# Optimization experiments

Measured on AMD Instinct MI355X. Metric: run time of the kernel, lower is better.

Reference implementation:

```python
import jax, jax.numpy as jnp
import numpy as np

B, C, H, W = 64, 3, 64, 64
F = 96          # base_filters
K = 8           # n_mixtures
h, w = H // 2, W // 2
C0 = 2 * C      # channels of each checkerboard half
SECTIONS = [C0, C0, C0 * K, C0 * K, C0 * K]
SPLITS = [int(s) for s in np.cumsum(SECTIONS)[:-1]]
EPS = 1e-6


def conv2d(x, wgt, b):
    y = jax.lax.conv_general_dilated(x, wgt, (1, 1), 'SAME',
                                     dimension_numbers=('NCHW', 'OIHW', 'NCHW'))
    return y + b[None, :, None, None]


def layer_norm(x, g, b, eps=1e-5):
    # nn.LayerNorm(mid_shape): normalize over (C,H,W) per sample
    mu = jnp.mean(x, axis=(1, 2, 3), keepdims=True)
    var = jnp.var(x, axis=(1, 2, 3), keepdims=True)
    return (x - mu) / jnp.sqrt(var + eps) * g[None] + b[None]


def checker_split(z, odd=False):
    Bz, Cz, Hz, Wz = z.shape
    z = z.reshape(Bz, Cz, Hz // 2, 2, Wz // 2, 2)
    p00 = z[:, :, :, 0, :, 0]; p01 = z[:, :, :, 0, :, 1]
    p10 = z[:, :, :, 1, :, 0]; p11 = z[:, :, :, 1, :, 1]
    z0 = jnp.concatenate([p00, p11], axis=1)  # even checkerboard
    z1 = jnp.concatenate([p01, p10], axis=1)  # odd checkerboard
    if odd:
        z0, z1 = z1, z0
    return z0, z1


def checker_merge(z0, z1, odd=False):
    if odd:
        z0, z1 = z1, z0
    Cz = z0.shape[1] // 2
    p00, p11 = z0[:, :Cz], z0[:, Cz:]
    p01, p10 = z1[:, :Cz], z1[:, Cz:]
    Bz, _, hz, wz = p00.shape
    zi = jnp.stack([jnp.stack([p00, p01], axis=-1),
                    jnp.stack([p10, p11], axis=-1)], axis=-2)  # (B,C,h,w,2i,2j)
    z = zi.transpose(0, 1, 2, 4, 3, 5).reshape(Bz, Cz, 2 * hz, 2 * wz)
    return z


def gated_attn(x, qkv_w, qkv_b, proj_w, proj_b):
    Bx, Fx, hx, wx = x.shape
    xf = x.reshape(Bx, Fx, hx * wx).transpose(0, 2, 1)  # (B, L, F)
    qkv = xf @ qkv_w.T + qkv_b
    q, k, v = jnp.split(qkv, 3, axis=-1)
    scores = jnp.einsum('bqf,bkf->bqk', q, k) / jnp.sqrt(jnp.float32(Fx))
    attn = jax.nn.softmax(scores, axis=-1)
    o = jnp.einsum('bqk,bkf->bqf', attn, v)
    g = o @ proj_w.T + proj_b
    ga, gb = jnp.split(g, 2, axis=-1)
    out = xf + ga * jax.nn.sigmoid(gb)  # gated residual
    return out.transpose(0, 2, 1).reshape(Bx, Fx, hx, wx)


def conditioner(z1, conv1_w, conv1_b, gconv_w, gconv_b, ln1_g, ln1_b,
                qkv_w, qkv_b, proj_w, proj_b, ln2_g, ln2_b, conv2_w, conv2_b):
    x = conv2d(z1, conv1_w, conv1_b)
    g = conv2d(x, gconv_w, gconv_b)
    ga, gb = jnp.split(g, 2, axis=1)
    x = x + ga * jax.nn.sigmoid(gb)          # GatedConv2d
    x = layer_norm(x, ln1_g, ln1_b)
    x = gated_attn(x, qkv_w, qkv_b, proj_w, proj_b)
    x = layer_norm(x, ln2_g, ln2_b)
    return conv2d(x, conv2_w, conv2_b)


def _forward(z, log_df_dz, conv1_w, conv1_b, gconv_w, gconv_b, ln1_g, ln1_b,
             qkv_w, qkv_b, proj_w, proj_b, ln2_g, ln2_b, conv2_w, conv2_b,
             a_log_scale, a_bias):
    z0, z1 = checker_split(z)
    params = conditioner(z1, conv1_w, conv1_b, gconv_w, gconv_b, ln1_g, ln1_b,
                         qkv_w, qkv_b, proj_w, proj_b, ln2_g, ln2_b, conv2_w, conv2_b)
    a, b, logpi, mu, s = jnp.split(params, SPLITS, axis=1)
    a = jnp.tanh(a) * a_log_scale + a_bias
    Bz = z0.shape[0]
    logpi = jax.nn.log_softmax(logpi.reshape(Bz, K, C0, h, w), axis=1)
    mu = mu.reshape(Bz, K, C0, h, w)
    s = s.reshape(Bz, K, C0, h, w)
    # mixture-of-logistics CDF
    u = (z0[:, None] - mu) * jnp.exp(-s)
    x = jnp.sum(jnp.exp(logpi) * jax.nn.sigmoid(u), axis=1)
    log_pdf = jax.scipy.special.logsumexp(
        logpi - s + jax.nn.log_sigmoid(u) + jax.nn.log_sigmoid(-u), axis=1)
    log_df_dz = log_df_dz + jnp.sum(log_pdf.reshape(Bz, -1), axis=1)
    # logit transform
    x = jnp.clip(x, EPS, 1.0 - EPS)
    z0n = jnp.log(x) - jnp.log1p(-x)
    log_df_dz = log_df_dz + jnp.sum((-jnp.log(x) - jnp.log1p(-x)).reshape(Bz, -1), axis=1)
    # affine rescale
    z0n = z0n * jnp.exp(a) + b
    log_df_dz = log_df_dz + jnp.sum(a.reshape(Bz, -1), axis=1)
    return checker_merge(z0n, z1), log_df_dz


def setup_inputs() -> dict:
    key = jax.random.key(0)
    ks = jax.random.split(key, 10)
    sc = 0.05
    return dict(
        z=jax.random.normal(ks[0], (B, C, H, W), jnp.float32),
        log_df_dz=jnp.zeros((B,), jnp.float32),
        conv1_w=sc * jax.random.normal(ks[1], (F, C0, 3, 3), jnp.float32),
        conv1_b=jnp.zeros((F,), jnp.float32),
        gconv_w=sc * jax.random.normal(ks[2], (2 * F, F, 3, 3), jnp.float32),
        gconv_b=jnp.zeros((2 * F,), jnp.float32),
        ln1_g=jnp.ones((F, h, w), jnp.float32),
        ln1_b=jnp.zeros((F, h, w), jnp.float32),
        qkv_w=sc * jax.random.normal(ks[3], (3 * F, F), jnp.float32),
        qkv_b=jnp.zeros((3 * F,), jnp.float32),
        proj_w=sc * jax.random.normal(ks[4], (2 * F, F), jnp.float32),
        proj_b=jnp.zeros((2 * F,), jnp.float32),
        ln2_g=jnp.ones((F, h, w), jnp.float32),
        ln2_b=jnp.zeros((F, h, w), jnp.float32),
        conv2_w=sc * jax.random.normal(ks[5], (sum(SECTIONS), F, 3, 3), jnp.float32),
        conv2_b=jnp.zeros((sum(SECTIONS),), jnp.float32),
        a_log_scale=0.01 * jax.random.normal(ks[6], (1,), jnp.float32),
        a_bias=0.01 * jax.random.normal(ks[7], (1,), jnp.float32),
    )


def reference(z, log_df_dz, conv1_w, conv1_b, gconv_w, gconv_b, ln1_g, ln1_b,
              qkv_w, qkv_b, proj_w, proj_b, ln2_g, ln2_b, conv2_w, conv2_b,
              a_log_scale, a_bias):
    return _forward(z, log_df_dz, conv1_w, conv1_b, gconv_w, gconv_b, ln1_g, ln1_b,
                    qkv_w, qkv_b, proj_w, proj_b, ln2_g, ln2_b, conv2_w, conv2_b,
                    a_log_scale, a_bias)
```

## Files before the change

### kernel.cpp

```cpp
#include <hip/hip_runtime.h>
#include <cstdint>
#include <cstddef>


typedef unsigned short u16;
typedef __attribute__((ext_vector_type(8))) short short8;
typedef __attribute__((ext_vector_type(4))) float f32x4;
typedef __attribute__((ext_vector_type(4))) unsigned int u32x4;

__device__ __forceinline__ float sigm(float x){ return 1.0f/(1.0f+__expf(-x)); }

__device__ __forceinline__ u16 f2bf(float f){
    unsigned int u = __float_as_uint(f);
    u += 0x7fffu + ((u >> 16) & 1u);
    return (u16)(u >> 16);
}
__device__ __forceinline__ float bf2f(u16 v){
    unsigned int u = ((unsigned int)v) << 16;
    return __uint_as_float(u);
}

__device__ __forceinline__ void dma16(const u16* g, u16* l){
    __builtin_amdgcn_global_load_lds(
        (const __attribute__((address_space(1))) void*)g,
        (__attribute__((address_space(3))) void*)l,
        16, 0, 0);
}

__device__ __forceinline__ float ex2(float x){
    float r; asm("v_exp_f32 %0, %1" : "=v"(r) : "v"(x)); return r;
}
__device__ __forceinline__ unsigned cvtpk(float lo, float hi){
    unsigned r; asm("v_cvt_pk_bf16_f32 %0, %1, %2" : "=v"(r) : "v"(lo), "v"(hi)); return r;
}
__device__ __forceinline__ void plswap32(unsigned &a, unsigned &b){
    asm("v_permlane32_swap_b32 %0, %1" : "+v"(a), "+v"(b));
}
__device__ __forceinline__ void plswap16(unsigned &a, unsigned &b){
    asm("v_permlane16_swap_b32 %0, %1" : "+v"(a), "+v"(b));
}

#define SOFTPACK(S, LACC, PA) do { \
    unsigned pk_[4][2]; \
    _Pragma("unroll") \
    for (int t=0;t<4;++t){ \
        float e0 = ex2(S[t][0]); \
        float e1 = ex2(S[t][1]); \
        float e2 = ex2(S[t][2]); \
        float e3 = ex2(S[t][3]); \
        LACC += (e0+e1)+(e2+e3); \
        pk_[t][0] = cvtpk(e0,e1); \
        pk_[t][1] = cvtpk(e2,e3); \
    } \
    _Pragma("unroll") \
    for (int kk=0;kk<2;++kk){ \
        unsigned a0 = pk_[2*kk][0], b0 = pk_[2*kk+1][0]; \
        unsigned a1 = pk_[2*kk][1], b1 = pk_[2*kk+1][1]; \
        plswap32(a0,b0); plswap16(a0,b0); \
        plswap32(a1,b1); plswap16(a1,b1); \
        u32x4 dw_; dw_[0]=a0; dw_[1]=a1; dw_[2]=b0; dw_[3]=b1; \
        PA[kk] = __builtin_bit_cast(short8, dw_); \
    } \
} while(0)

__device__ __forceinline__ short8 ln_frag(const u16* __restrict__ xg,
    const float* __restrict__ gt, const float* __restrict__ bt,
    int p, int c0, float mu, float rr)
{
    short8 x8 = *reinterpret_cast<const short8*>(xg + (size_t)p*96 + c0);
    const float* gp = gt + (size_t)p*96 + c0;
    const float* bp = bt + (size_t)p*96 + c0;
    short8 o;
    #pragma unroll
    for (int j=0;j<8;++j){
        float ag = rr*gp[j];
        o[j] = (short)f2bf(bf2f((u16)x8[j])*ag + (bp[j] - mu*ag));
    }
    return o;
}

__global__ __launch_bounds__(256) void k_prep(
    const float* __restrict__ z, const float* __restrict__ c1w, const float* __restrict__ c1b,
    const float* __restrict__ gw, const float* __restrict__ c2w,
    const float* __restrict__ qkvw, const float* __restrict__ pw,
    const float* __restrict__ ln1g, const float* __restrict__ ln1b,
    const float* __restrict__ ln2g, const float* __restrict__ ln2b,
    const float* __restrict__ logdf,
    u16* __restrict__ x1b,
    u16* __restrict__ Wg, u16* __restrict__ W2,
    u16* __restrict__ Wqkv, u16* __restrict__ Wproj,
    float* __restrict__ gt1, float* __restrict__ bt1,
    float* __restrict__ gt2, float* __restrict__ bt2,
    float* __restrict__ outlog)
{
    int blk = blockIdx.x;
    int tid = threadIdx.x;
    __shared__ float tin[6][6][34];
    __shared__ __align__(16) u16 Wc[96][72];
    __shared__ __align__(16) u16 imc[128][72];

    if (blk < 512){
        int b  = blk >> 3;
        int pg = blk & 7;
        int r0 = pg*4;
        for (int e = tid; e < 96*72; e += 256){
            int oc = e/72, k = e%72;
            Wc[oc][k] = (k < 54) ? f2bf(c1w[oc*54 + k]) : (u16)0;
        }
        for (int idx = tid; idx < 6*6*34; idx += 256){
            int c = idx/204, rem = idx%204;
            int rr = rem/34, q = rem%34;
            int ii = r0 - 1 + rr, jj = q - 1;
            float v = 0.f;
            if ((unsigned)ii < 32u && (unsigned)jj < 32u){
                if (c < 3) v = z[((b*3+c)*64 + 2*ii)*64 + (2*jj+1)];
                else       v = z[((b*3+(c-3))*64 + (2*ii+1))*64 + 2*jj];
            }
            tin[c][rr][q] = v;
        }
        __syncthreads();
        for (int e = tid; e < 128*72; e += 256){
            int px = e/72, k = e%72;
            float v = 0.f;
            if (k < 54){
                int c = k/9, rr = (k%9)/3, dcc = k%3;
                v = tin[c][(px>>5)+rr][(px&31)+dcc];
            }
            imc[px][k] = f2bf(v);
        }
        __syncthreads();

        int w = tid >> 6, lane = tid & 63;
        int cc = lane & 15, gg = lane >> 4;
        f32x4 acc[2][6];
        #pragma unroll
        for (int u=0;u<2;++u)
            #pragma unroll
            for (int t=0;t<6;++t) acc[u][t] = (f32x4){0.f,0.f,0.f,0.f};

        #pragma unroll
        for (int ks=0; ks<2; ++ks){
            short8 a0 = *reinterpret_cast<const short8*>(&imc[w*32 + cc     ][ks*32 + 8*gg]);
            short8 a1 = *reinterpret_cast<const short8*>(&imc[w*32 + 16 + cc][ks*32 + 8*gg]);
            #pragma unroll
            for (int t=0; t<6; ++t){
                short8 bb = *reinterpret_cast<const short8*>(&Wc[t*16+cc][ks*32 + 8*gg]);
                acc[0][t] = __builtin_amdgcn_mfma_f32_16x16x32_bf16(a0, bb, acc[0][t], 0,0,0);
                acc[1][t] = __builtin_amdgcn_mfma_f32_16x16x32_bf16(a1, bb, acc[1][t], 0,0,0);
            }
        }

        #pragma unroll
        for (int u=0;u<2;++u){
            int p0 = pg*128 + w*32 + u*16 + gg*4;
            #pragma unroll
            for (int t=0;t<6;++t){
                int oc = t*16+cc;
                float bv = c1b[oc];
                #pragma unroll
                for (int r=0;r<4;++r)
                    x1b[((size_t)(b*1024) + p0 + r)*96 + oc] = f2bf(acc[u][t][r] + bv);
            }
        }
    } else if (blk < 1160){
        int idx = (blk-512)*256 + tid;
        int j = idx & 7;
        int lane = (idx >> 3) & 63;
        int fo = idx >> 9;
        int frag = fo % 18;
        int tob = fo / 18;
        int obk = tob & 1, tap = tob >> 1;
        int t = frag/3, ks = frag%3;
        int cc = lane & 15, gg = lane >> 4;
        int ocp = obk*96 + t*16 + cc;
        int r2 = ocp%96, isB = r2/48, i2 = r2%48;
        int oc = (ocp/96)*48 + i2 + isB*96;
        int ic = ks*32 + 8*gg + j;
        Wg[idx] = f2bf(gw[(size_t)(oc*96+ic)*9 + tap]);
    } else if (blk < 1700){
        int idx = (blk-1160)*256 + tid;
        int j = idx & 7;
        int lane = (idx >> 3) & 63;
        int fo = idx >> 9;
        int frag = fo % 15;
        int tob = fo / 15;
        int obk = tob & 1, tap = tob >> 1;
        int t = frag/3, ks = frag%3;
        int cc = lane & 15, gg = lane >> 4;
        int oc = obk*80 + t*16 + cc;
        int ic = ks*32 + 8*gg + j;
        W2[idx] = (oc < 156) ? f2bf(c2w[(size_t)(oc*96+ic)*9 + tap]) : (u16)0;
    } else if (blk < 1808){
        int idx = (blk-1700)*256 + tid;
        int j = idx & 7;
        int lane = (idx >> 3) & 63;
        int fo = idx >> 9;
        int frag = fo % 27;
        int obk = fo / 27;
        int t = frag/3, ks = frag%3;
        int cc = lane & 15, gg = lane >> 4;
        int n = obk*144 + t*16 + cc;
        int ic = ks*32 + 8*gg + j;
        Wqkv[idx] = f2bf(qkvw[(size_t)n*96 + ic]);
    } else if (blk < 1880){
        int idx = (blk-1808)*256 + tid;
        int j = idx & 7;
        int lane = (idx >> 3) & 63;
        int fo = idx >> 9;
        int frag = fo % 18;
        int obk = fo / 18;
        int t = frag/3, ks = frag%3;
        int cc = lane & 15, gg = lane >> 4;
        int ocp = obk*96 + t*16 + cc;
        int r2 = ocp%96, isB = r2/48, i2 = r2%48;
        int oc = obk*48 + i2 + isB*96;
        int ic = ks*32 + 8*gg + j;
        Wproj[idx] = f2bf(pw[(size_t)oc*96 + ic]);
    } else if (blk < 2264){
        int idx = (blk-1880)*256 + tid;
        int c = idx >> 10, p = idx & 1023;
        gt1[p*96 + c] = ln1g[idx];
    } else if (blk < 2648){
        int idx = (blk-2264)*256 + tid;
        int c = idx >> 10, p = idx & 1023;
        bt1[p*96 + c] = ln1b[idx];
    } else if (blk < 3032){
        int idx = (blk-2648)*256 + tid;
        int c = idx >> 10, p = idx & 1023;
        gt2[p*96 + c] = ln2g[idx];
    } else if (blk < 3416){
        int idx = (blk-3032)*256 + tid;
        int c = idx >> 10, p = idx & 1023;
        bt2[p*96 + c] = ln2b[idx];
    } else {
        if (tid < 64) outlog[tid] = logdf[tid];
    }
}

__global__ __launch_bounds__(256,4) void k_gconv(const u16* __restrict__ Xpb,
    const u16* __restrict__ Wt, const float* __restrict__ bias,
    u16* __restrict__ outb, float* __restrict__ partials)
{
    int blk  = blockIdx.x;
    int obk  = blk & 1;
    int pblk = (blk >> 1) & 7;
    int b    = blk >> 4;
    int tid  = threadIdx.x;
    int w = tid >> 6, lane = tid & 63;
    int cc = lane & 15, gg = lane >> 4;

    __shared__ __align__(16) u16 Ws[2][9216];
    __shared__ float red[8];

    f32x4 acc[2][6];
    #pragma unroll
    for (int u=0;u<2;++u)
        #pragma unroll
        for (int t=0;t<6;++t) acc[u][t] = (f32x4){0.f,0.f,0.f,0.f};

    int base = pblk*128 + w*32;
    int ia = base >> 5;
    const u16* xb = Xpb + (size_t)b*1024*96;

    {
        const u16* src = Wt + (size_t)obk*9216;
        #pragma unroll
        for (int i=0;i<5;++i){
            int c = tid + 256*i;
            if (c < 1152) dma16(src + (size_t)c*8, Ws[0] + (size_t)(w*64+256*i)*8);
        }
    }

    for (int tap=0; tap<9; ++tap){
        __syncthreads();
        if (tap < 8){
            const u16* src = Wt + (size_t)((tap+1)*2 + obk)*9216;
            int nb = (tap+1)&1;
            #pragma unroll
            for (int i=0;i<5;++i){
                int c = tid + 256*i;
                if (c < 1152) dma16(src + (size_t)c*8, Ws[nb] + (size_t)(w*64+256*i)*8);
            }
        }
        const u16* Wc = Ws[tap&1];
        int dr = tap/3 - 1, dc = tap%3 - 1;

        int ii = ia + dr;
        int jj0 = cc + dc, jj1 = cc + 16 + dc;
        bool rv = ((unsigned)ii < 32u);
        bool v0 = rv && ((unsigned)jj0 < 32u);
        bool v1 = rv && ((unsigned)jj1 < 32u);
        const u16* ar0 = xb + (ptrdiff_t)(ii*32 + jj0)*96 + 8*gg;
        const u16* ar1 = xb + (ptrdiff_t)(ii*32 + jj1)*96 + 8*gg;

        #pragma unroll
        for (int ks=0; ks<3; ++ks){
            short8 a0 = {0,0,0,0,0,0,0,0};
            short8 a1 = {0,0,0,0,0,0,0,0};
            if (v0) a0 = *reinterpret_cast<const short8*>(ar0 + ks*32);
            if (v1) a1 = *reinterpret_cast<const short8*>(ar1 + ks*32);
            #pragma unroll
            for (int t=0; t<6; ++t){
                short8 bb = *reinterpret_cast<const short8*>(Wc + ((size_t)(t*3+ks)*64 + lane)*8);
                acc[0][t] = __builtin_amdgcn_mfma_f32_16x16x32_bf16(a0, bb, acc[0][t], 0,0,0);
                acc[1][t] = __builtin_amdgcn_mfma_f32_16x16x32_bf16(a1, bb, acc[1][t], 0,0,0);
            }
        }
    }

    float s = 0.f, ssq = 0.f;
    #pragma unroll
    for (int u=0;u<2;++u){
        int p0 = base + u*16 + gg*4;
        #pragma unroll
        for (int t=0;t<3;++t){
            int ocA = obk*48 + t*16+cc;
            float ba = bias[ocA], bbv = bias[ocA+96];
            #pragma unroll
            for (int r=0;r<4;++r){
                float res = bf2f(Xpb[((size_t)b*1024 + p0+r)*96 + ocA]);
                float va = acc[u][t][r]   + ba;
                float vb = acc[u][t+3][r] + bbv;
                float v = res + va*sigm(vb);
                outb[((size_t)b*1024 + p0+r)*96 + ocA] = f2bf(v);
                s += v; ssq += v*v;
            }
        }
    }
    #pragma unroll
    for (int o=32;o>0;o>>=1){ s += __shfl_down(s,o,64); ssq += __shfl_down(ssq,o,64); }
    if (lane==0){ red[w]=s; red[4+w]=ssq; }
    __syncthreads();
    if (tid==0){
        int slot = b*16 + pblk*2 + obk;
        partials[slot*2+0] = red[0]+red[1]+red[2]+red[3];
        partials[slot*2+1] = red[4]+red[5]+red[6]+red[7];
    }
}

__global__ __launch_bounds__(256) void k_lne(const u16* __restrict__ xb,
    const float* __restrict__ gt, const float* __restrict__ bt,
    const float* __restrict__ partials, u16* __restrict__ out)
{
    int b = blockIdx.x / 48, rem = blockIdx.x % 48;
    float s=0.f, ss=0.f;
    #pragma unroll
    for (int i=0;i<16;++i){ s += partials[(b*16+i)*2]; ss += partials[(b*16+i)*2+1]; }
    float mu = s/98304.f;
    float r = rsqrtf(ss/98304.f - mu*mu + 1e-5f);

    int e8 = rem*256 + threadIdx.x;
    size_t base = (size_t)b*98304 + (size_t)e8*8;
    short8 x8 = *reinterpret_cast<const short8*>(xb + base);
    const float* gp = gt + e8*8;
    const float* bp = bt + e8*8;
    short8 o8;
    #pragma unroll
    for (int i=0;i<8;++i)
        o8[i] = (short)f2bf((bf2f((u16)x8[i]) - mu)*r*gp[i] + bp[i]);
    *reinterpret_cast<short8*>(out + base) = o8;
}

__global__ __launch_bounds__(256,4) void k_qkvm(const u16* __restrict__ Xg,
    const float* __restrict__ gt, const float* __restrict__ bt,
    const float* __restrict__ part,
    const u16* __restrict__ Wt, const float* __restrict__ bias,
    u16* __restrict__ Qb, u16* __restrict__ Kf, u16* __restrict__ Vf)
{
    int blk  = blockIdx.x;
    int obk  = blk & 1;
    int pblk = (blk >> 1) & 7;
    int b    = blk >> 4;
    int tid  = threadIdx.x;
    int w = tid >> 6, lane = tid & 63;
    int cc = lane & 15, gg = lane >> 4;
    const float scale = 0.14724445f;

    __shared__ __align__(16) u16 Ws[13824];
    {
        const u16* src = Wt + (size_t)obk*13824;
        #pragma unroll
        for (int i=0;i<7;++i){
            int c = tid + 256*i;
            if (c < 1728) dma16(src + (size_t)c*8, Ws + (size_t)(w*64+256*i)*8);
        }
    }

    float sS=0.f, sQ=0.f;
    #pragma unroll
    for (int i=0;i<16;++i){ sS += part[(b*16+i)*2]; sQ += part[(b*16+i)*2+1]; }
    float mu = sS/98304.f;
    float rr = rsqrtf(sQ/98304.f - mu*mu + 1e-5f);

    f32x4 acc[2][9];
    #pragma unroll
    for (int u=0;u<2;++u)
        #pragma unroll
        for (int t=0;t<9;++t) acc[u][t] = (f32x4){0.f,0.f,0.f,0.f};

    int base = pblk*128 + w*32;
    const u16* xg = Xg + (size_t)b*1024*96;
    __syncthreads();

    #pragma unroll
    for (int ks=0; ks<3; ++ks){
        int c0 = ks*32 + 8*gg;
        short8 a0 = ln_frag(xg, gt, bt, base+cc,    c0, mu, rr);
        short8 a1 = ln_frag(xg, gt, bt, base+cc+16, c0, mu, rr);
        #pragma unroll
        for (int t=0; t<9; ++t){
            short8 bb = *reinterpret_cast<const short8*>(Ws + ((size_t)(t*3+ks)*64 + lane)*8);
            acc[0][t] = __builtin_amdgcn_mfma_f32_16x16x32_bf16(a0, bb, acc[0][t], 0,0,0);
            acc[1][t] = __builtin_amdgcn_mfma_f32_16x16x32_bf16(a1, bb, acc[1][t], 0,0,0);
        }
    }

    #pragma unroll
    for (int u=0;u<2;++u){
        int p0 = base + u*16 + gg*4;
        #pragma unroll
        for (int t=0;t<9;++t){
            int n = obk*144 + t*16+cc;
            float bv = bias[n];
            #pragma unroll
            for (int r=0;r<4;++r){
                int p = p0 + r;
                float av = acc[u][t][r] + bv;
                if (n < 96){
                    Qb[((size_t)(b*1024+p))*96 + n] = f2bf(av*scale);
                } else if (n < 192){
                    int f = n-96;
                    int jt = p>>6, t16 = (p>>4)&3, ccs = p&15;
                    int ks = f>>5, ggs = (f>>3)&3, j = f&7;
                    Kf[(size_t)(b*16+jt)*6144 + (size_t)(((t16*3+ks)*4+ggs)*16+ccs)*8 + j] = f2bf(av);
                } else {
                    int f = n-192;
                    int jt = p>>6, kl = p&63;
                    int kk = kl>>5, ggs = (kl>>3)&3, j = kl&7;
                    int ft = f>>4, ccs = f&15;
                    Vf[(size_t)(b*16+jt)*6144 + (size_t)(((ft*2+kk)*4+ggs)*16+ccs)*8 + j] = f2bf(av);
                }
            }
        }
    }
}

__global__ __launch_bounds__(256,2) void k_attn(const u16* __restrict__ Qb,
    const u16* __restrict__ Kf, const u16* __restrict__ Vf, u16* __restrict__ Ob)
{
    int qt = blockIdx.x >> 6;
    int b  = blockIdx.x & 63;
    int tid = threadIdx.x;
    int w  = tid >> 6;
    int lane = tid & 63;
    int cc = lane & 15;
    int gg = lane >> 4;

    __shared__ __align__(16) u16 Ks[3][6144];
    __shared__ __align__(16) u16 Vs[3][6144];

    int q0 = qt*128 + w*32;

    short8 qf[2][3];
    {
        const u16* qr0 = Qb + ((size_t)(b*1024 + q0 + cc))*96;
        #pragma unroll
        for (int ks=0; ks<3; ++ks){
            qf[0][ks] = *reinterpret_cast<const short8*>(qr0 + ks*32 + 8*gg);
            qf[1][ks] = *reinterpret_cast<const short8*>(qr0 + (size_t)16*96 + ks*32 + 8*gg);
        }
    }

    f32x4 Oacc[2][6];
    #pragma unroll
    for (int u=0;u<2;++u)
        #pragma unroll
        for (int ft=0; ft<6; ++ft) Oacc[u][ft] = (f32x4){0.f,0.f,0.f,0.f};
    float l_acc[2] = {0.f, 0.f};

    const u16* Kb0 = Kf + (size_t)(b*16)*6144;
    const u16* Vb0 = Vf + (size_t)(b*16)*6144;

    #pragma unroll
    for (int i=0;i<3;++i){
        size_t c8 = (size_t)(tid + 256*i)*8;
        size_t l8 = (size_t)(w*64 + 256*i)*8;
        dma16(Kb0 + c8, Ks[0] + l8);
        dma16(Vb0 + c8, Vs[0] + l8);
    }
    #pragma unroll
    for (int i=0;i<3;++i){
        size_t c8 = (size_t)(6144 + (tid + 256*i)*8);
        size_t l8 = (size_t)(w*64 + 256*i)*8;
        dma16(Kb0 + c8, Ks[1] + l8);
        dma16(Vb0 + c8, Vs[1] + l8);
    }

    for (int jt=0; jt<16; ++jt){
        if (jt < 15) asm volatile("s_waitcnt vmcnt(6)" ::: "memory");
        else         asm volatile("s_waitcnt vmcnt(0)" ::: "memory");
        __builtin_amdgcn_s_barrier();
        __builtin_amdgcn_sched_barrier(0);

        if (jt < 14){
            const u16* kn = Kb0 + (size_t)(jt+2)*6144;
            const u16* vn = Vb0 + (size_t)(jt+2)*6144;
            u16* kd = Ks[(jt+2)%3];
            u16* vd = Vs[(jt+2)%3];
            #pragma unroll
            for (int i=0;i<3;++i){
                size_t c8 = (size_t)(tid + 256*i)*8;
                size_t l8 = (size_t)(w*64 + 256*i)*8;
                dma16(kn + c8, kd + l8);
                dma16(vn + c8, vd + l8);
            }
        }

        const u16* Kc = Ks[jt%3];
        const u16* Vc = Vs[jt%3];

        f32x4 S0[4], S1[4];
        #pragma unroll
        for (int t=0;t<4;++t){ S0[t] = (f32x4){0.f,0.f,0.f,0.f}; S1[t] = (f32x4){0.f,0.f,0.f,0.f}; }

        __builtin_amdgcn_s_setprio(1);
        #pragma unroll
        for (int ks=0; ks<3; ++ks){
            #pragma unroll
            for (int t=0; t<4; ++t){
                short8 kb = *reinterpret_cast<const short8*>(Kc + ((t*3+ks)*64 + lane)*8);
                S0[t] = __builtin_amdgcn_mfma_f32_16x16x32_bf16(kb, qf[0][ks], S0[t], 0,0,0);
                S1[t] = __builtin_amdgcn_mfma_f32_16x16x32_bf16(kb, qf[1][ks], S1[t], 0,0,0);
            }
        }
        __builtin_amdgcn_s_setprio(0);

        short8 pa0[2], pa1[2];
        SOFTPACK(S0, l_acc[0], pa0);
        SOFTPACK(S1, l_acc[1], pa1);

        __builtin_amdgcn_s_setprio(1);
        #pragma unroll
        for (int kk=0; kk<2; ++kk){
            #pragma unroll
            for (int ft=0; ft<6; ++ft){
                short8 vb = *reinterpret_cast<const short8*>(Vc + ((ft*2+kk)*64 + lane)*8);
                Oacc[0][ft] = __builtin_amdgcn_mfma_f32_16x16x32_bf16(pa0[kk], vb, Oacc[0][ft], 0,0,0);
                Oacc[1][ft] = __builtin_amdgcn_mfma_f32_16x16x32_bf16(pa1[kk], vb, Oacc[1][ft], 0,0,0);
            }
        }
        __builtin_amdgcn_s_setprio(0);
    }

    #pragma unroll
    for (int u=0;u<2;++u){
        float lv = l_acc[u];
        lv += __shfl_xor(lv, 16, 64);
        lv += __shfl_xor(lv, 32, 64);
        float linv[4];
        #pragma unroll
        for (int r=0;r<4;++r) linv[r] = 1.0f / __shfl(lv, 4*gg + r, 64);
        #pragma unroll
        for (int ft=0; ft<6; ++ft)
            #pragma unroll
            for (int r=0; r<4; ++r)
                Ob[((size_t)(b*1024 + q0 + u*16 + 4*gg + r))*96 + ft*16 + cc]
                    = f2bf(Oacc[u][ft][r]*linv[r]);
    }
}

__global__ __launch_bounds__(256,4) void k_projm(const u16* __restrict__ Opb,
    const u16* __restrict__ Wt, const float* __restrict__ bias,
    const u16* __restrict__ Xg, const float* __restrict__ gt, const float* __restrict__ bt,
    const float* __restrict__ part1,
    u16* __restrict__ outb, float* __restrict__ partials)
{
    int blk  = blockIdx.x;
    int obk  = blk & 1;
    int pblk = (blk >> 1) & 7;
    int b    = blk >> 4;
    int tid  = threadIdx.x;
    int w = tid >> 6, lane = tid & 63;
    int cc = lane & 15, gg = lane >> 4;

    __shared__ __align__(16) u16 Ws[9216];
    __shared__ float red[8];
    {
        const u16* src = Wt + (size_t)obk*9216;
        #pragma unroll
        for (int i=0;i<5;++i){
            int c = tid + 256*i;
            if (c < 1152) dma16(src + (size_t)c*8, Ws + (size_t)(w*64+256*i)*8);
        }
    }

    float sS=0.f, sQ=0.f;
    #pragma unroll
    for (int i=0;i<16;++i){ sS += part1[(b*16+i)*2]; sQ += part1[(b*16+i)*2+1]; }
    float mu1 = sS/98304.f;
    float rr1 = rsqrtf(sQ/98304.f - mu1*mu1 + 1e-5f);

    f32x4 acc[2][6];
    #pragma unroll
    for (int u=0;u<2;++u)
        #pragma unroll
        for (int t=0;t<6;++t) acc[u][t] = (f32x4){0.f,0.f,0.f,0.f};

    int base = pblk*128 + w*32;
    const u16* xb = Opb + ((size_t)b*1024 + base)*96;
    __syncthreads();

    #pragma unroll
    for (int ks=0; ks<3; ++ks){
        short8 a0 = *reinterpret_cast<const short8*>(xb + (size_t)cc*96      + ks*32 + 8*gg);
        short8 a1 = *reinterpret_cast<const short8*>(xb + (size_t)(cc+16)*96 + ks*32 + 8*gg);
        #pragma unroll
        for (int t=0; t<6; ++t){
            short8 bb = *reinterpret_cast<const short8*>(Ws + ((size_t)(t*3+ks)*64 + lane)*8);
            acc[0][t] = __builtin_amdgcn_mfma_f32_16x16x32_bf16(a0, bb, acc[0][t], 0,0,0);
            acc[1][t] = __builtin_amdgcn_mfma_f32_16x16x32_bf16(a1, bb, acc[1][t], 0,0,0);
        }
    }

    const u16* resb = Xg + (size_t)b*1024*96;
    float s = 0.f, ssq = 0.f;
    #pragma unroll
    for (int u=0;u<2;++u){
        int p0 = base + u*16 + gg*4;
        #pragma unroll
        for (int t=0;t<3;++t){
            int ocA = obk*48 + t*16+cc;
            float ba = bias[ocA], bbv = bias[ocA+96];
            #pragma unroll
            for (int r=0;r<4;++r){
                int pl = p0 + r;
                float ga = acc[u][t][r]   + ba;
                float gb = acc[u][t+3][r] + bbv;
                float xv = bf2f(resb[(size_t)pl*96 + ocA]);
                float res = (xv - mu1)*rr1*gt[(size_t)pl*96 + ocA] + bt[(size_t)pl*96 + ocA];
                float v = res + ga * sigm(gb);
                outb[((size_t)b*1024 + pl)*96 + ocA] = f2bf(v);
                s += v; ssq += v*v;
            }
        }
    }
    #pragma unroll
    for (int o=32;o>0;o>>=1){ s += __shfl_down(s,o,64); ssq += __shfl_down(ssq,o,64); }
    if (lane==0){ red[w]=s; red[4+w]=ssq; }
    __syncthreads();
    if (tid==0){
        int slot = b*16 + pblk*2 + obk;
        partials[slot*2+0] = red[0]+red[1]+red[2]+red[3];
        partials[slot*2+1] = red[4]+red[5]+red[6]+red[7];
    }
}

__global__ __launch_bounds__(256,2) void k_c2mix(const u16* __restrict__ Xpb,
    const u16* __restrict__ Wt, const float* __restrict__ bias,
    const float* __restrict__ z, const float* __restrict__ a_ls_p,
    const float* __restrict__ a_b_p, float* __restrict__ out_z, float* __restrict__ out_log)
{
    int blk  = blockIdx.x;
    int pblk = blk & 7;
    int b    = blk >> 3;
    int tid  = threadIdx.x;
    int w = tid >> 6, lane = tid & 63;
    int cc = lane & 15, gg = lane >> 4;

    __shared__ __align__(16) u16 SM[30720];
    __shared__ float red[4];

    f32x4 acc[2][10];
    #pragma unroll
    for (int u=0;u<2;++u)
        #pragma unroll
        for (int t=0;t<10;++t) acc[u][t] = (f32x4){0.f,0.f,0.f,0.f};

    int base = pblk*128 + w*32;
    int ia = base >> 5;
    const u16* xb = Xpb + (size_t)b*1024*96;

    {
        #pragma unroll
        for (int i=0;i<8;++i){
            int c = tid + 256*i;
            if (c < 1920) dma16(Wt + (size_t)c*8, SM + (size_t)(w*64+256*i)*8);
        }
    }

    for (int tap=0; tap<9; ++tap){
        __syncthreads();
        if (tap < 8){
            const u16* src = Wt + (size_t)(tap+1)*15360;
            u16* dst = SM + (size_t)((tap+1)&1)*15360;
            #pragma unroll
            for (int i=0;i<8;++i){
                int c = tid + 256*i;
                if (c < 1920) dma16(src + (size_t)c*8, dst + (size_t)(w*64+256*i)*8);
            }
        }
        const u16* Wc = SM + (size_t)(tap&1)*15360;
        int dr = tap/3 - 1, dc = tap%3 - 1;

        int ii = ia + dr;
        int jj0 = cc + dc, jj1 = cc + 16 + dc;
        bool rv = ((unsigned)ii < 32u);
        bool v0 = rv && ((unsigned)jj0 < 32u);
        bool v1 = rv && ((unsigned)jj1 < 32u);
        const u16* ar0 = xb + (ptrdiff_t)(ii*32 + jj0)*96 + 8*gg;
        const u16* ar1 = xb + (ptrdiff_t)(ii*32 + jj1)*96 + 8*gg;

        #pragma unroll
        for (int ks=0; ks<3; ++ks){
            short8 a0 = {0,0,0,0,0,0,0,0};
            short8 a1 = {0,0,0,0,0,0,0,0};
            if (v0) a0 = *reinterpret_cast<const short8*>(ar0 + ks*32);
            if (v1) a1 = *reinterpret_cast<const short8*>(ar1 + ks*32);
            #pragma unroll
            for (int t=0; t<10; ++t){
                int fl = (t<5) ? (t*3+ks) : (15 + (t-5)*3 + ks);
                short8 bb = *reinterpret_cast<const short8*>(Wc + ((size_t)fl*64 + lane)*8);
                acc[0][t] = __builtin_amdgcn_mfma_f32_16x16x32_bf16(a0, bb, acc[0][t], 0,0,0);
                acc[1][t] = __builtin_amdgcn_mfma_f32_16x16x32_bf16(a1, bb, acc[1][t], 0,0,0);
            }
        }
    }

    __syncthreads();
    #pragma unroll
    for (int u=0;u<2;++u){
        int lp0 = w*32 + u*16 + gg*4;
        #pragma unroll
        for (int t=0;t<10;++t){
            int oc = (t<5) ? (t*16+cc) : (80 + (t-5)*16 + cc);
            if (oc < 156){
                float bv = bias[oc];
                #pragma unroll
                for (int r=0;r<4;++r)
                    SM[oc*132 + lp0 + r] = f2bf(acc[u][t][r] + bv);
            }
        }
    }
    __syncthreads();

    float als = a_ls_p[0], abv = a_b_p[0];
    float logsum = 0.f;
    #pragma unroll
    for (int e3=0;e3<3;++e3){
        int e  = tid + 256*e3;
        int c0 = e >> 7, xp = e & 127;
        int pix = pblk*128 + xp;
        int i = pix >> 5, j = pix & 31;

        if (c0 < 3){
            int idx01 = ((b*3+c0)*64 + 2*i)*64 + 2*j+1;
            int idx10 = ((b*3+c0)*64 + 2*i+1)*64 + 2*j;
            out_z[idx01] = z[idx01];
            out_z[idx10] = z[idx10];
        }

        float z0v = (c0<3) ? z[((b*3+c0)*64 + 2*i)*64 + 2*j]
                           : z[((b*3+(c0-3))*64 + 2*i+1)*64 + 2*j+1];
        float a_raw = bf2f(SM[(c0)*132 + xp]);
        float bco   = bf2f(SM[(6+c0)*132 + xp]);
        float lpk[8], muk[8], svk[8];
        float m1 = -1e30f;
        #pragma unroll
        for (int k=0;k<8;++k){
            lpk[k] = bf2f(SM[(12 + k*6 + c0)*132 + xp]);
            muk[k] = bf2f(SM[(60 + k*6 + c0)*132 + xp]);
            svk[k] = bf2f(SM[(108 + k*6 + c0)*132 + xp]);
            m1 = fmaxf(m1, lpk[k]);
        }
        float se = 0.f;
        #pragma unroll
        for (int k=0;k<8;++k) se += __expf(lpk[k]-m1);
        float lse = m1 + __logf(se);
        float xm = 0.f, mt = -1e30f;
        float tk[8];
        #pragma unroll
        for (int k=0;k<8;++k){
            float lpn = lpk[k] - lse;
            float u = (z0v - muk[k]) * __expf(-svk[k]);
            float au = fabsf(u);
            xm += __expf(lpn) * (1.f/(1.f+__expf(-u)));
            float lss = -(au + 2.f*log1pf(__expf(-au)));
            float t2 = lpn - svk[k] + lss;
            tk[k] = t2; mt = fmaxf(mt, t2);
        }
        float se2 = 0.f;
        #pragma unroll
        for (int k=0;k<8;++k) se2 += __expf(tk[k]-mt);
        float logacc = mt + __logf(se2);
        xm = fminf(fmaxf(xm, 1e-6f), 1.f-1e-6f);
        float lx = __logf(xm), l1x = log1pf(-xm);
        logacc += -lx - l1x;
        float aa = tanhf(a_raw)*als + abv;
        float z0n = (lx - l1x)*__expf(aa) + bco;
        logacc += aa;
        int oidx = (c0<3) ? ((b*3+c0)*64 + 2*i)*64 + 2*j
                          : ((b*3+(c0-3))*64 + 2*i+1)*64 + 2*j+1;
        out_z[oidx] = z0n;
        logsum += logacc;
    }

    #pragma unroll
    for (int o=32;o>0;o>>=1) logsum += __shfl_down(logsum, o, 64);
    if (lane==0) red[w] = logsum;
    __syncthreads();
    if (tid==0) atomicAdd(out_log + b, red[0]+red[1]+red[2]+red[3]);
}

extern "C" void kernel_launch(void* const* d_in, const int* in_sizes, int n_in,
                              void* d_out, int out_size, void* d_ws, size_t ws_size,
                              hipStream_t stream)
{
    const float* z     = (const float*)d_in[0];
    const float* logdf = (const float*)d_in[1];
    const float* c1w   = (const float*)d_in[2];
    const float* c1b   = (const float*)d_in[3];
    const float* gw    = (const float*)d_in[4];
    const float* gcb   = (const float*)d_in[5];
    const float* ln1g  = (const float*)d_in[6];
    const float* ln1b  = (const float*)d_in[7];
    const float* qkvw  = (const float*)d_in[8];
    const float* qkvb  = (const float*)d_in[9];
    const float* pw    = (const float*)d_in[10];
    const float* pbb   = (const float*)d_in[11];
    const float* ln2g  = (const float*)d_in[12];
    const float* ln2b  = (const float*)d_in[13];
    const float* c2w   = (const float*)d_in[14];
    const float* c2b   = (const float*)d_in[15];
    const float* als   = (const float*)d_in[16];
    const float* ab    = (const float*)d_in[17];

    float* out_z   = (float*)d_out;
    float* out_log = out_z + 786432;

    float* ws     = (float*)d_ws;
    u16*   x1b    = (u16*)(ws + 0);
    u16*   xg_b   = (u16*)(ws + 3145728);
    u16*   Kf     = (u16*)(ws + 6291456);
    u16*   Vf     = (u16*)(ws + 9437184);
    u16*   Ob     = (u16*)(ws + 12582912);
    u16*   x2b    = (u16*)(ws + 15728640);
    u16*   Qb     = x1b;
    u16*   xln2b  = Kf;
    const size_t T = 19660800;
    float* gt1    = ws + T;
    float* bt1    = ws + T + 98304;
    float* gt2    = ws + T + 196608;
    float* bt2    = ws + T + 294912;
    float* part1  = ws + T + 393216;
    float* part2  = ws + T + 395264;
    u16*   Wg     = (u16*)(ws + T + 397568);
    u16*   W2     = (u16*)(ws + T + 480512);
    u16*   Wqkv   = (u16*)(ws + T + 549632);
    u16*   Wproj  = (u16*)(ws + T + 563456);

    k_prep   <<<3417, 256, 0, stream>>>(z, c1w, c1b, gw, c2w, qkvw, pw,
                                        ln1g, ln1b, ln2g, ln2b, logdf,
                                        x1b, Wg, W2, Wqkv, Wproj,
                                        gt1, bt1, gt2, bt2, out_log);
    k_gconv  <<<1024, 256, 0, stream>>>(x1b, Wg, gcb, xg_b, part1);
    k_qkvm   <<<1024, 256, 0, stream>>>(xg_b, gt1, bt1, part1, Wqkv, qkvb, Qb, Kf, Vf);
    k_attn   <<<512, 256, 0, stream>>>(Qb, Kf, Vf, Ob);
    k_projm  <<<1024, 256, 0, stream>>>(Ob, Wproj, pbb, xg_b, gt1, bt1, part1, x2b, part2);
    k_lne    <<<3072, 256, 0, stream>>>(x2b, gt2, bt2, part2, xln2b);
    k_c2mix  <<<512,  256, 0, stream>>>(xln2b, W2, c2b, z, als, ab, out_z, out_log);
}
```

Measured before the change: 256.2 us.

## Fuse attention with gated output projection and residual layernorm epilogue

Merges the attention kernel and the projection/gating kernel into one. The normalized attention output tile is kept in LDS (padded rows) instead of written to global and reread, and shared memory is reused for the full projection weight after the K/V loop. Each block now computes both output halves, so it holds 24 accumulator tiles and emits two partial-sum slots. This removes one launch and the global round trip of the attention output, but raises register pressure and serializes the projection behind the attention tail.

Result: faster. 247.0 us (median of 3 runs) (-3.6%).

```diff
diff --git a/kernel.cpp b/kernel.cpp
--- a/kernel.cpp
+++ b/kernel.cpp
@@ -445,8 +445,12 @@
     }
 }
 
-__global__ __launch_bounds__(256,2) void k_attn(const u16* __restrict__ Qb,
-    const u16* __restrict__ Kf, const u16* __restrict__ Vf, u16* __restrict__ Ob)
+__global__ __launch_bounds__(256,2) void k_attnproj(const u16* __restrict__ Qb,
+    const u16* __restrict__ Kf, const u16* __restrict__ Vf,
+    const u16* __restrict__ Wpg, const float* __restrict__ pbias,
+    const u16* __restrict__ Xg, const float* __restrict__ gt, const float* __restrict__ bt,
+    const float* __restrict__ part1,
+    u16* __restrict__ outb, float* __restrict__ partials)
 {
     int qt = blockIdx.x >> 6;
     int b  = blockIdx.x & 63;
@@ -456,8 +460,19 @@
     int cc = lane & 15;
     int gg = lane >> 4;
 
-    __shared__ __align__(16) u16 Ks[3][6144];
-    __shared__ __align__(16) u16 Vs[3][6144];
+    __shared__ __align__(16) u16 SM[36864];
+    __shared__ float red[16];
+
+    u16* Ksb = SM;
+    u16* Vsb = SM + 18432;
+    u16* Wp  = SM;
+    u16* Ot  = SM + 18432;
+
+    float sS=0.f, sQ=0.f;
+    #pragma unroll
+    for (int i=0;i<16;++i){ sS += part1[(b*16+i)*2]; sQ += part1[(b*16+i)*2+1]; }
+    float mu1 = sS/98304.f;
+    float rr1 = rsqrtf(sQ/98304.f - mu1*mu1 + 1e-5f);
 
     int q0 = qt*128 + w*32;
 
@@ -485,15 +500,15 @@
     for (int i=0;i<3;++i){
         size_t c8 = (size_t)(tid + 256*i)*8;
         size_t l8 = (size_t)(w*64 + 256*i)*8;
-        dma16(Kb0 + c8, Ks[0] + l8);
-        dma16(Vb0 + c8, Vs[0] + l8);
+        dma16(Kb0 + c8, Ksb + l8);
+        dma16(Vb0 + c8, Vsb + l8);
     }
     #pragma unroll
     for (int i=0;i<3;++i){
         size_t c8 = (size_t)(6144 + (tid + 256*i)*8);
         size_t l8 = (size_t)(w*64 + 256*i)*8;
-        dma16(Kb0 + c8, Ks[1] + l8);
-        dma16(Vb0 + c8, Vs[1] + l8);
+        dma16(Kb0 + c8, Ksb + 6144 + l8);
+        dma16(Vb0 + c8, Vsb + 6144 + l8);
     }
 
     for (int jt=0; jt<16; ++jt){
@@ -505,8 +520,8 @@
         if (jt < 14){
             const u16* kn = Kb0 + (size_t)(jt+2)*6144;
             const u16* vn = Vb0 + (size_t)(jt+2)*6144;
-            u16* kd = Ks[(jt+2)%3];
-            u16* vd = Vs[(jt+2)%3];
+            u16* kd = Ksb + (size_t)((jt+2)%3)*6144;
+            u16* vd = Vsb + (size_t)((jt+2)%3)*6144;
             #pragma unroll
             for (int i=0;i<3;++i){
                 size_t c8 = (size_t)(tid + 256*i)*8;
@@ -516,8 +531,8 @@
             }
         }
 
-        const u16* Kc = Ks[jt%3];
-        const u16* Vc = Vs[jt%3];
+        const u16* Kc = Ksb + (size_t)(jt%3)*6144;
+        const u16* Vc = Vsb + (size_t)(jt%3)*6144;
 
         f32x4 S0[4], S1[4];
         #pragma unroll
@@ -550,6 +565,14 @@
             }
         }
         __builtin_amdgcn_s_setprio(0);
+    }
+
+    __syncthreads();
+
+    #pragma unroll
+    for (int i=0;i<9;++i){
+        int c = tid + 256*i;
+        dma16(Wpg + (size_t)c*8, Wp + (size_t)(w*64+256*i)*8);
     }
 
     #pragma unroll
@@ -564,94 +587,69 @@
         for (int ft=0; ft<6; ++ft)
             #pragma unroll
             for (int r=0; r<4; ++r)
-                Ob[((size_t)(b*1024 + q0 + u*16 + 4*gg + r))*96 + ft*16 + cc]
+                Ot[(size_t)(w*32 + u*16 + 4*gg + r)*104 + ft*16 + cc]
                     = f2bf(Oacc[u][ft][r]*linv[r]);
     }
-}
-
-__global__ __launch_bounds__(256,4) void k_projm(const u16* __restrict__ Opb,
-    const u16* __restrict__ Wt, const float* __restrict__ bias,
-    const u16* __restrict__ Xg, const float* __restrict__ gt, const float* __restrict__ bt,
-    const float* __restrict__ part1,
-    u16* __restrict__ outb, float* __restrict__ partials)
-{
-    int blk  = blockIdx.x;
-    int obk  = blk & 1;
-    int pblk = (blk >> 1) & 7;
-    int b    = blk >> 4;
-    int tid  = threadIdx.x;
-    int w = tid >> 6, lane = tid & 63;
-    int cc = lane & 15, gg = lane >> 4;
-
-    __shared__ __align__(16) u16 Ws[9216];
-    __shared__ float red[8];
-    {
-        const u16* src = Wt + (size_t)obk*9216;
-        #pragma unroll
-        for (int i=0;i<5;++i){
-            int c = tid + 256*i;
-            if (c < 1152) dma16(src + (size_t)c*8, Ws + (size_t)(w*64+256*i)*8);
-        }
-    }
-
-    float sS=0.f, sQ=0.f;
-    #pragma unroll
-    for (int i=0;i<16;++i){ sS += part1[(b*16+i)*2]; sQ += part1[(b*16+i)*2+1]; }
-    float mu1 = sS/98304.f;
-    float rr1 = rsqrtf(sQ/98304.f - mu1*mu1 + 1e-5f);
-
-    f32x4 acc[2][6];
+
+    __syncthreads();
+
+    f32x4 pacc[2][12];
     #pragma unroll
     for (int u=0;u<2;++u)
         #pragma unroll
-        for (int t=0;t<6;++t) acc[u][t] = (f32x4){0.f,0.f,0.f,0.f};
-
-    int base = pblk*128 + w*32;
-    const u16* xb = Opb + ((size_t)b*1024 + base)*96;
-    __syncthreads();
+        for (int t=0;t<12;++t) pacc[u][t] = (f32x4){0.f,0.f,0.f,0.f};
 
     #pragma unroll
     for (int ks=0; ks<3; ++ks){
-        short8 a0 = *reinterpret_cast<const short8*>(xb + (size_t)cc*96      + ks*32 + 8*gg);
-        short8 a1 = *reinterpret_cast<const short8*>(xb + (size_t)(cc+16)*96 + ks*32 + 8*gg);
-        #pragma unroll
-        for (int t=0; t<6; ++t){
-            short8 bb = *reinterpret_cast<const short8*>(Ws + ((size_t)(t*3+ks)*64 + lane)*8);
-            acc[0][t] = __builtin_amdgcn_mfma_f32_16x16x32_bf16(a0, bb, acc[0][t], 0,0,0);
-            acc[1][t] = __builtin_amdgcn_mfma_f32_16x16x32_bf16(a1, bb, acc[1][t], 0,0,0);
+        short8 a0 = *reinterpret_cast<const short8*>(Ot + (size_t)(w*32 + cc     )*104 + ks*32 + 8*gg);
+        short8 a1 = *reinterpret_cast<const short8*>(Ot + (size_t)(w*32 + cc + 16)*104 + ks*32 + 8*gg);
+        #pragma unroll
+        for (int t2=0; t2<12; ++t2){
+            int obk = t2/6, tl = t2%6;
+            short8 bb = *reinterpret_cast<const short8*>(Wp + ((size_t)(obk*18 + tl*3 + ks)*64 + lane)*8);
+            pacc[0][t2] = __builtin_amdgcn_mfma_f32_16x16x32_bf16(a0, bb, pacc[0][t2], 0,0,0);
+            pacc[1][t2] = __builtin_amdgcn_mfma_f32_16x16x32_bf16(a1, bb, pacc[1][t2], 0,0,0);
         }
     }
 
     const u16* resb = Xg + (size_t)b*1024*96;
-    float s = 0.f, ssq = 0.f;
+    float s0=0.f, q0s=0.f, s1=0.f, q1s=0.f;
     #pragma unroll
     for (int u=0;u<2;++u){
-        int p0 = base + u*16 + gg*4;
-        #pragma unroll
-        for (int t=0;t<3;++t){
-            int ocA = obk*48 + t*16+cc;
-            float ba = bias[ocA], bbv = bias[ocA+96];
-            #pragma unroll
-            for (int r=0;r<4;++r){
-                int pl = p0 + r;
-                float ga = acc[u][t][r]   + ba;
-                float gb = acc[u][t+3][r] + bbv;
-                float xv = bf2f(resb[(size_t)pl*96 + ocA]);
-                float res = (xv - mu1)*rr1*gt[(size_t)pl*96 + ocA] + bt[(size_t)pl*96 + ocA];
-                float v = res + ga * sigm(gb);
-                outb[((size_t)b*1024 + pl)*96 + ocA] = f2bf(v);
-                s += v; ssq += v*v;
-            }
-        }
-    }
-    #pragma unroll
-    for (int o=32;o>0;o>>=1){ s += __shfl_down(s,o,64); ssq += __shfl_down(ssq,o,64); }
-    if (lane==0){ red[w]=s; red[4+w]=ssq; }
+        int p0 = qt*128 + w*32 + u*16 + gg*4;
+        #pragma unroll
+        for (int obk=0;obk<2;++obk){
+            #pragma unroll
+            for (int tl=0;tl<3;++tl){
+                int ocA = obk*48 + tl*16 + cc;
+                float ba = pbias[ocA], bbv = pbias[ocA+96];
+                #pragma unroll
+                for (int r=0;r<4;++r){
+                    int pl = p0 + r;
+                    float ga = pacc[u][obk*6+tl][r]   + ba;
+                    float gb = pacc[u][obk*6+tl+3][r] + bbv;
+                    float xv = bf2f(resb[(size_t)pl*96 + ocA]);
+                    float res = (xv - mu1)*rr1*gt[(size_t)pl*96 + ocA] + bt[(size_t)pl*96 + ocA];
+                    float v = res + ga * sigm(gb);
+                    outb[((size_t)b*1024 + pl)*96 + ocA] = f2bf(v);
+                    if (obk==0){ s0 += v; q0s += v*v; } else { s1 += v; q1s += v*v; }
+                }
+            }
+        }
+    }
+    #pragma unroll
+    for (int o=32;o>0;o>>=1){
+        s0 += __shfl_down(s0,o,64);  q0s += __shfl_down(q0s,o,64);
+        s1 += __shfl_down(s1,o,64);  q1s += __shfl_down(q1s,o,64);
+    }
+    if (lane==0){ red[w*4+0]=s0; red[w*4+1]=q0s; red[w*4+2]=s1; red[w*4+3]=q1s; }
     __syncthreads();
     if (tid==0){
-        int slot = b*16 + pblk*2 + obk;
-        partials[slot*2+0] = red[0]+red[1]+red[2]+red[3];
-        partials[slot*2+1] = red[4]+red[5]+red[6]+red[7];
+        int slot = b*16 + qt*2;
+        partials[(size_t)slot*2+0]     = red[0]+red[4]+red[8]+red[12];
+        partials[(size_t)slot*2+1]     = red[1]+red[5]+red[9]+red[13];
+        partials[(size_t)(slot+1)*2+0] = red[2]+red[6]+red[10]+red[14];
+        partials[(size_t)(slot+1)*2+1] = red[3]+red[7]+red[11]+red[15];
     }
 }
 
@@ -842,7 +840,6 @@
     u16*   xg_b   = (u16*)(ws + 3145728);
     u16*   Kf     = (u16*)(ws + 6291456);
     u16*   Vf     = (u16*)(ws + 9437184);
-    u16*   Ob     = (u16*)(ws + 12582912);
     u16*   x2b    = (u16*)(ws + 15728640);
     u16*   Qb     = x1b;
     u16*   xln2b  = Kf;
@@ -858,14 +855,14 @@
     u16*   Wqkv   = (u16*)(ws + T + 549632);
     u16*   Wproj  = (u16*)(ws + T + 563456);
 
-    k_prep   <<<3417, 256, 0, stream>>>(z, c1w, c1b, gw, c2w, qkvw, pw,
-                                        ln1g, ln1b, ln2g, ln2b, logdf,
-                                        x1b, Wg, W2, Wqkv, Wproj,
-                                        gt1, bt1, gt2, bt2, out_log);
-    k_gconv  <<<1024, 256, 0, stream>>>(x1b, Wg, gcb, xg_b, part1);
-    k_qkvm   <<<1024, 256, 0, stream>>>(xg_b, gt1, bt1, part1, Wqkv, qkvb, Qb, Kf, Vf);
-    k_attn   <<<512, 256, 0, stream>>>(Qb, Kf, Vf, Ob);
-    k_projm  <<<1024, 256, 0, stream>>>(Ob, Wproj, pbb, xg_b, gt1, bt1, part1, x2b, part2);
-    k_lne    <<<3072, 256, 0, stream>>>(x2b, gt2, bt2, part2, xln2b);
-    k_c2mix  <<<512,  256, 0, stream>>>(xln2b, W2, c2b, z, als, ab, out_z, out_log);
-}
+    k_prep     <<<3417, 256, 0, stream>>>(z, c1w, c1b, gw, c2w, qkvw, pw,
+                                          ln1g, ln1b, ln2g, ln2b, logdf,
+                                          x1b, Wg, W2, Wqkv, Wproj,
+                                          gt1, bt1, gt2, bt2, out_log);
+    k_gconv    <<<1024, 256, 0, stream>>>(x1b, Wg, gcb, xg_b, part1);
+    k_qkvm     <<<1024, 256, 0, stream>>>(xg_b, gt1, bt1, part1, Wqkv, qkvb, Qb, Kf, Vf);
+    k_attnproj <<<512,  256, 0, stream>>>(Qb, Kf, Vf, Wproj, pbb,
+                                          xg_b, gt1, bt1, part1, x2b, part2);
+    k_lne      <<<3072, 256, 0, stream>>>(x2b, gt2, bt2, part2, xln2b);
+    k_c2mix    <<<512,  256, 0, stream>>>(xln2b, W2, c2b, z, als, ab, out_z, out_log);
+}
```
